# Optimization experiments

Measured on AMD Instinct MI355X. Metric: run time of the kernel, lower is better.

Reference implementation:

```python
import jax, jax.numpy as jnp
import numpy as np

N_NODES = 20000
N_EDGES = 640000
HIDDEN = 128
HEADS = 8
HEAD_DIM = HIDDEN // HEADS
SCALE = HEAD_DIM ** -0.5
EPS = 1e-8


def setup_inputs() -> dict:
    key = jax.random.key(0)
    ks = jax.random.split(key, 12)
    s = HIDDEN ** -0.5
    return {
        "query": jax.random.normal(ks[0], (N_NODES, HIDDEN), jnp.float32),
        "key": jax.random.normal(ks[1], (N_NODES, HIDDEN), jnp.float32),
        "value": jax.random.normal(ks[2], (N_NODES, HIDDEN), jnp.float32),
        "edge_index": jax.random.randint(ks[3], (2, N_EDGES), 0, N_NODES, jnp.int64 if jax.config.jax_enable_x64 else jnp.int32),
        "Wq": jax.random.normal(ks[4], (HIDDEN, HIDDEN), jnp.float32) * s,
        "bq": jax.random.normal(ks[5], (HIDDEN,), jnp.float32) * s,
        "Wk": jax.random.normal(ks[6], (HIDDEN, HIDDEN), jnp.float32) * s,
        "bk": jax.random.normal(ks[7], (HIDDEN,), jnp.float32) * s,
        "Wv": jax.random.normal(ks[8], (HIDDEN, HIDDEN), jnp.float32) * s,
        "bv": jax.random.normal(ks[9], (HIDDEN,), jnp.float32) * s,
        "Wo": jax.random.normal(ks[10], (HIDDEN, HIDDEN), jnp.float32) * s,
        "bo": jax.random.normal(ks[11], (HIDDEN,), jnp.float32) * s,
    }


def reference(query, key, value, edge_index, Wq, bq, Wk, bk, Wv, bv, Wo, bo):
    n = query.shape[0]
    # projections (torch nn.Linear: x @ W.T + b)
    Q = (query @ Wq.T + bq).reshape(n, HEADS, HEAD_DIM)
    K = (key @ Wk.T + bk).reshape(n, HEADS, HEAD_DIM)
    V = (value @ Wv.T + bv).reshape(n, HEADS, HEAD_DIM)

    src, dst = edge_index[0], edge_index[1]
    # per-edge, per-head scores: [E, H]
    scores = jnp.einsum('ehd,ehd->eh', Q[dst], K[src]) * SCALE
    # segment softmax over incoming edges of each dst node
    seg_max = jax.ops.segment_max(scores, dst, num_segments=n)  # [N, H]
    seg_max = jnp.where(jnp.isfinite(seg_max), seg_max, 0.0)
    exp_scores = jnp.exp(scores - seg_max[dst])
    seg_sum = jax.ops.segment_sum(exp_scores, dst, num_segments=n)  # [N, H]
    attn = exp_scores / (seg_sum[dst] + EPS)  # [E, H]

    # scatter-weighted aggregation of V[src] into dst
    weighted = attn[:, :, None] * V[src]  # [E, H, D]
    out = jax.ops.segment_sum(weighted, dst, num_segments=n)  # [N, H, D]
    out = out.reshape(n, HIDDEN)
    return out @ Wo.T + bo
```

## Files before the change

### kernel.cpp

```cpp
#include <hip/hip_runtime.h>
#include <math.h>

#define NN 20000
#define NE 640000
#define HID 128
#define NH 8
#define HD 16
#define ATT_SCALE 0.25f

#define EPB 4096
#define NBLK1 157
#define NBUCK 157
#define SCAN_N (NBUCK * NBLK1)
#define SPT 25
#define PCHUNK 79

typedef __attribute__((ext_vector_type(8))) short bhalf8;
typedef __attribute__((ext_vector_type(4))) float floatx4;

__device__ __forceinline__ short f2b(float f) {
  union { float f; unsigned u; } a;
  a.f = f;
  unsigned r = a.u + 0x7FFF + ((a.u >> 16) & 1);
  return (short)(r >> 16);
}

__device__ __forceinline__ float b2f(short s) {
  union { unsigned u; float f; } a;
  a.u = ((unsigned)(unsigned short)s) << 16;
  return a.f;
}

__device__ __forceinline__ bhalf8 load_a8(const float* __restrict__ p) {
  float4 x0 = *(const float4*)p;
  float4 x1 = *(const float4*)(p + 4);
  bhalf8 a;
  a[0] = f2b(x0.x); a[1] = f2b(x0.y); a[2] = f2b(x0.z); a[3] = f2b(x0.w);
  a[4] = f2b(x1.x); a[5] = f2b(x1.y); a[6] = f2b(x1.z); a[7] = f2b(x1.w);
  return a;
}

__global__ __launch_bounds__(256) void k_hist_wconv(
    const int* __restrict__ dst, int* __restrict__ cnt1,
    const float* __restrict__ W0, const float* __restrict__ W1,
    const float* __restrict__ W2, const float* __restrict__ W3,
    short* __restrict__ out) {
  int t = threadIdx.x, b = blockIdx.x;
  if (b < NBLK1) {
    __shared__ int h[NBUCK];
    for (int i = t; i < NBUCK; i += 256) h[i] = 0;
    __syncthreads();
    const int4* d4 = (const int4*)dst;
    int q0 = (b * EPB) >> 2;
#pragma unroll
    for (int it = 0; it < EPB / 1024; ++it) {
      int i4 = q0 + it * 256 + t;
      if (i4 < NE / 4) {
        int4 d = d4[i4];
        atomicAdd(&h[d.x >> 7], 1);
        atomicAdd(&h[d.y >> 7], 1);
        atomicAdd(&h[d.z >> 7], 1);
        atomicAdd(&h[d.w >> 7], 1);
      }
    }
    __syncthreads();
    for (int i = t; i < NBUCK; i += 256) cnt1[i * NBLK1 + b] = h[i];
  } else {
    int i = (b - NBLK1) * 1024 + t * 4;
    int m = i >> 14;
    const float* src = (m == 0) ? W0 : (m == 1) ? W1 : (m == 2) ? W2 : W3;
    float4 x = *(const float4*)(src + (i & 16383));
    short4 o;
    o.x = f2b(x.x); o.y = f2b(x.y); o.z = f2b(x.z); o.w = f2b(x.w);
    *(short4*)(out + i) = o;
  }
}

template <int STRIDE, int HALF>
__device__ __forceinline__ void gemm_mfma(const float* __restrict__ X,
                                          const short* __restrict__ Wb,
                                          const float* __restrict__ B,
                                          short* __restrict__ O, int wrow) {
  int lane = threadIdx.x & 63;
  int rr = lane & 15;
  int g = lane >> 4;
  int arow = wrow + rr;
  floatx4 acc[8];
#pragma unroll
  for (int nt = 0; nt < 8; ++nt) acc[nt] = (floatx4){0.f, 0.f, 0.f, 0.f};
#pragma unroll
  for (int kt = 0; kt < 4; ++kt) {
    bhalf8 a;
    if (arow < NN) {
      a = load_a8(X + (size_t)arow * HID + kt * 32 + g * 8);
    } else {
      a = (bhalf8){0, 0, 0, 0, 0, 0, 0, 0};
    }
#pragma unroll
    for (int nt = 0; nt < 8; ++nt) {
      bhalf8 b = *(const bhalf8*)(Wb + (nt * 16 + rr) * HID + kt * 32 + g * 8);
      acc[nt] = __builtin_amdgcn_mfma_f32_16x16x32_bf16(a, b, acc[nt], 0, 0, 0);
    }
  }
  int orow0 = wrow + g * 4;
#pragma unroll
  for (int nt = 0; nt < 8; ++nt) {
    int col = nt * 16 + rr;
    float bias = B[col];
#pragma unroll
    for (int i = 0; i < 4; ++i) {
      int r = orow0 + i;
      if (r < NN) {
        O[((size_t)(nt >> 1) * NN + r) * STRIDE + HALF + (nt & 1) * 16 + rr] =
            f2b(acc[nt][i] + bias);
      }
    }
  }
}

__global__ __launch_bounds__(1024) void k_scan_proj(
    int* __restrict__ cnt1, int* __restrict__ boff,
    const float* __restrict__ q, const float* __restrict__ k,
    const float* __restrict__ v, const short* __restrict__ Wb,
    const float* __restrict__ bq, const float* __restrict__ bk,
    const float* __restrict__ bv, short* __restrict__ Qh,
    short* __restrict__ KVh) {
  __shared__ int sa[1024], sb[1024];
  int t = threadIdx.x;
  if (blockIdx.x == 0) {
    int base = t * SPT;
    int s = 0;
#pragma unroll 5
    for (int u = 0; u < SPT; ++u) {
      int i = base + u;
      s += (i < SCAN_N) ? cnt1[i] : 0;
    }
    sa[t] = s;
    __syncthreads();
    int* sp = sa;
    int* dp = sb;
    for (int st = 1; st < 1024; st <<= 1) {
      dp[t] = sp[t] + (t >= st ? sp[t - st] : 0);
      __syncthreads();
      int* tmp = sp; sp = dp; dp = tmp;
    }
    int run = sp[t] - s;
#pragma unroll 5
    for (int u = 0; u < SPT; ++u) {
      int i = base + u;
      if (i < SCAN_N) {
        int vv = cnt1[i];
        cnt1[i] = run;
        run += vv;
      }
    }
    __syncthreads();
    for (int i = t; i < NBUCK; i += 1024) boff[i] = cnt1[i * NBLK1];
    if (t == 0) boff[NBUCK] = NE;
  } else {
    int b = blockIdx.x - 1;
    int mat = b / PCHUNK;
    int wrow = (b % PCHUNK) * 256 + (t >> 6) * 16;
    if (mat == 0) gemm_mfma<32, 0>(q, Wb, bq, Qh, wrow);
    else if (mat == 1) gemm_mfma<64, 0>(k, Wb + 16384, bk, KVh, wrow);
    else gemm_mfma<64, 32>(v, Wb + 2 * 16384, bv, KVh, wrow);
  }
}

__global__ __launch_bounds__(256) void k_p1scat(const int* __restrict__ src,
                                                const int* __restrict__ dst,
                                                const int* __restrict__ cnt1,
                                                int* __restrict__ tmp) {
  __shared__ int cur[NBUCK];
  int t = threadIdx.x, b = blockIdx.x;
  for (int i = t; i < NBUCK; i += 256) cur[i] = cnt1[i * NBLK1 + b];
  __syncthreads();
  const int4* s4 = (const int4*)src;
  const int4* d4 = (const int4*)dst;
  int q0 = (b * EPB) >> 2;
#pragma unroll
  for (int it = 0; it < EPB / 1024; ++it) {
    int i4 = q0 + it * 256 + t;
    if (i4 < NE / 4) {
      int4 s = s4[i4];
      int4 d = d4[i4];
      int p;
      p = atomicAdd(&cur[d.x >> 7], 1); tmp[p] = (s.x << 7) | (d.x & 127);
      p = atomicAdd(&cur[d.y >> 7], 1); tmp[p] = (s.y << 7) | (d.y & 127);
      p = atomicAdd(&cur[d.z >> 7], 1); tmp[p] = (s.z << 7) | (d.z & 127);
      p = atomicAdd(&cur[d.w >> 7], 1); tmp[p] = (s.w << 7) | (d.w & 127);
    }
  }
}

__global__ __launch_bounds__(128, 4) void k_edge(
    const int* __restrict__ tmp, const int* __restrict__ boff,
    const short* __restrict__ Qh, const short* __restrict__ KVh,
    const short* __restrict__ Wb, const float* __restrict__ bo,
    float* __restrict__ O) {
  __shared__ int hits[512];
  __shared__ int els[512];
  __shared__ short att[8][136];
  __shared__ int h8[8], c8[8], o8[8];
  __shared__ int nhit;
  int t = threadIdx.x;
  int bx = blockIdx.x;
  int b = bx >> 4;
  int l0 = (bx & 15) * 8;
  int node0 = 8 * bx;
  if (t < 8) h8[t] = 0;
  if (t == 0) nhit = 0;
  __syncthreads();
  int lo = boff[b], hi = boff[b + 1];
  const int4* t4 = (const int4*)tmp;
  int q0i = lo >> 2, q1i = (hi + 3) >> 2;
  for (int i4 = q0i + t; i4 < q1i; i4 += 128) {
    int4 w4 = t4[i4];
    int e = 4 * i4;
#pragma unroll
    for (int u = 0; u < 4; ++u) {
      int w = (u == 0) ? w4.x : (u == 1) ? w4.y : (u == 2) ? w4.z : w4.w;
      int ei = e + u;
      if (ei >= lo && ei < hi) {
        unsigned rel = (unsigned)((w & 127) - l0);
        if (rel < 8u) {
          int p = atomicAdd(&nhit, 1);
          if (p < 512) hits[p] = w;
          atomicAdd(&h8[rel], 1);
        }
      }
    }
  }
  __syncthreads();
  if (t == 0) {
    int r = 0;
#pragma unroll
    for (int u = 0; u < 8; ++u) {
      o8[u] = r;
      c8[u] = r;
      r += h8[u];
    }
  }
  __syncthreads();
  int n = nhit < 512 ? nhit : 512;
  for (int i = t; i < n; i += 128) {
    int w = hits[i];
    int p = atomicAdd(&c8[(w & 127) - l0], 1);
    els[p] = w >> 7;
  }
  __syncthreads();
  int nl = t >> 4;
  int node = node0 + nl;
  int sub = t & 15;
  int j = sub >> 2;
  int r = sub & 3;
  int i0 = o8[nl];
  int i1 = i0 + h8[nl];
  bool valid = node < NN;
#pragma unroll
  for (int hp = 0; hp < 4; ++hp) {
    float qf[8];
    if (valid) {
      bhalf8 qv = *(const bhalf8*)(Qh + ((size_t)hp * NN + node) * 32 + r * 8);
#pragma unroll
      for (int u = 0; u < 8; ++u) qf[u] = b2f(qv[u]);
    } else {
#pragma unroll
      for (int u = 0; u < 8; ++u) qf[u] = 0.f;
    }
    float l = 0.f;
    float acc[8];
#pragma unroll
    for (int u = 0; u < 8; ++u) acc[u] = 0.f;
    int i = i0 + j;
    for (; i + 4 < i1; i += 8) {
      int s1 = els[i], s2 = els[i + 4];
      const short* b1 = KVh + ((size_t)hp * NN + s1) * 64;
      const short* b2 = KVh + ((size_t)hp * NN + s2) * 64;
      bhalf8 kc1 = *(const bhalf8*)(b1 + r * 8);
      bhalf8 vc1 = *(const bhalf8*)(b1 + 32 + r * 8);
      bhalf8 kc2 = *(const bhalf8*)(b2 + r * 8);
      bhalf8 vc2 = *(const bhalf8*)(b2 + 32 + r * 8);
      float d1 = 0.f, d2 = 0.f;
#pragma unroll
      for (int u = 0; u < 8; ++u) {
        d1 += qf[u] * b2f(kc1[u]);
        d2 += qf[u] * b2f(kc2[u]);
      }
      d1 += __shfl_xor(d1, 1, 64);
      d2 += __shfl_xor(d2, 1, 64);
      float p1 = __expf(d1 * ATT_SCALE);
      float p2 = __expf(d2 * ATT_SCALE);
      l += p1 + p2;
#pragma unroll
      for (int u = 0; u < 8; ++u) acc[u] += p1 * b2f(vc1[u]) + p2 * b2f(vc2[u]);
    }
    if (i < i1) {
      int s1 = els[i];
      const short* b1 = KVh + ((size_t)hp * NN + s1) * 64;
      bhalf8 kc1 = *(const bhalf8*)(b1 + r * 8);
      bhalf8 vc1 = *(const bhalf8*)(b1 + 32 + r * 8);
      float d1 = 0.f;
#pragma unroll
      for (int u = 0; u < 8; ++u) d1 += qf[u] * b2f(kc1[u]);
      d1 += __shfl_xor(d1, 1, 64);
      float p1 = __expf(d1 * ATT_SCALE);
      l += p1;
#pragma unroll
      for (int u = 0; u < 8; ++u) acc[u] += p1 * b2f(vc1[u]);
    }
#pragma unroll
    for (int mask = 4; mask <= 8; mask <<= 1) {
      l += __shfl_xor(l, mask, 64);
#pragma unroll
      for (int u = 0; u < 8; ++u) acc[u] += __shfl_xor(acc[u], mask, 64);
    }
    float inv = 1.f / (l + 1e-8f);
    if (j == 0) {
      bhalf8 st;
#pragma unroll
      for (int u = 0; u < 8; ++u) st[u] = f2b(acc[u] * inv);
      *(bhalf8*)(&att[nl][hp * 32 + r * 8]) = st;
    }
  }
  __syncthreads();
  int w = t >> 6;
  int plane = t & 63;
  int rr = plane & 15;
  int pg = plane >> 4;
  const short* Wo = Wb + 3 * 16384;
  floatx4 oacc[4];
#pragma unroll
  for (int ntl = 0; ntl < 4; ++ntl) oacc[ntl] = (floatx4){0.f, 0.f, 0.f, 0.f};
#pragma unroll
  for (int kt = 0; kt < 4; ++kt) {
    bhalf8 a;
    if (rr < 8 && node0 + rr < NN) {
      a = *(const bhalf8*)(&att[rr][kt * 32 + pg * 8]);
    } else {
      a = (bhalf8){0, 0, 0, 0, 0, 0, 0, 0};
    }
#pragma unroll
    for (int ntl = 0; ntl < 4; ++ntl) {
      int nt = w * 4 + ntl;
      bhalf8 bb = *(const bhalf8*)(Wo + (nt * 16 + rr) * HID + kt * 32 + pg * 8);
      oacc[ntl] = __builtin_amdgcn_mfma_f32_16x16x32_bf16(a, bb, oacc[ntl], 0, 0, 0);
    }
  }
#pragma unroll
  for (int ntl = 0; ntl < 4; ++ntl) {
    int col = (w * 4 + ntl) * 16 + rr;
    float bias = bo[col];
#pragma unroll
    for (int ii = 0; ii < 4; ++ii) {
      int rw = pg * 4 + ii;
      if (rw < 8 && node0 + rw < NN) {
        O[(size_t)(node0 + rw) * HID + col] = oacc[ntl][ii] + bias;
      }
    }
  }
}

extern "C" void kernel_launch(void* const* d_in, const int* in_sizes, int n_in,
                              void* d_out, int out_size, void* d_ws,
                              size_t ws_size, hipStream_t stream) {
  const float* q = (const float*)d_in[0];
  const float* k = (const float*)d_in[1];
  const float* v = (const float*)d_in[2];
  const int* ei = (const int*)d_in[3];
  const float* Wq = (const float*)d_in[4];
  const float* bq = (const float*)d_in[5];
  const float* Wk = (const float*)d_in[6];
  const float* bk = (const float*)d_in[7];
  const float* Wv = (const float*)d_in[8];
  const float* bv = (const float*)d_in[9];
  const float* Wo = (const float*)d_in[10];
  const float* bo = (const float*)d_in[11];
  const int* src = ei;
  const int* dst = ei + NE;

  int* tmp = (int*)d_ws;
  int* cnt1 = tmp + NE;
  int* boff = cnt1 + 24704;
  short* Wb = (short*)(boff + 160);
  short* Qh = Wb + 4 * 16384;
  short* KVh = Qh + NN * HID;
  float* O = (float*)d_out;

  k_hist_wconv<<<NBLK1 + 64, 256, 0, stream>>>(dst, cnt1, Wq, Wk, Wv, Wo, Wb);
  k_scan_proj<<<1 + 3 * PCHUNK, 1024, 0, stream>>>(cnt1, boff, q, k, v, Wb, bq,
                                                   bk, bv, Qh, KVh);
  k_p1scat<<<NBLK1, 256, 0, stream>>>(src, dst, cnt1, tmp);
  k_edge<<<NBUCK * 16, 128, 0, stream>>>(tmp, boff, Qh, KVh, Wb, bo, O);
}
```

Baseline: 98.23 us.

## Bin edges by destination octet so each edge block reads only its own edges

Changes the counting sort from 128-node buckets to 8-node bins, matching the per-block node group of the edge kernel. A new column-scan kernel computes per-bin offsets across histogram blocks, and the edge kernel reads its contiguous edge range directly instead of filtering a shared bucket. This removes the redundant scanning of each large bucket by sixteen blocks. It adds a larger histogram in shared memory and global memory, plus an extra launch whose serial per-bin loop reads memory with a stride.

```diff
diff --git a/kernel.cpp b/kernel.cpp
--- a/kernel.cpp
+++ b/kernel.cpp
@@ -10,9 +10,8 @@
 
 #define EPB 4096
 #define NBLK1 157
-#define NBUCK 157
-#define SCAN_N (NBUCK * NBLK1)
-#define SPT 25
+#define FBIN 2500
+#define SPT2 3
 #define PCHUNK 79
 
 typedef __attribute__((ext_vector_type(8))) short bhalf8;
@@ -47,8 +46,8 @@
     short* __restrict__ out) {
   int t = threadIdx.x, b = blockIdx.x;
   if (b < NBLK1) {
-    __shared__ int h[NBUCK];
-    for (int i = t; i < NBUCK; i += 256) h[i] = 0;
+    __shared__ int h[FBIN];
+    for (int i = t; i < FBIN; i += 256) h[i] = 0;
     __syncthreads();
     const int4* d4 = (const int4*)dst;
     int q0 = (b * EPB) >> 2;
@@ -57,14 +56,14 @@
       int i4 = q0 + it * 256 + t;
       if (i4 < NE / 4) {
         int4 d = d4[i4];
-        atomicAdd(&h[d.x >> 7], 1);
-        atomicAdd(&h[d.y >> 7], 1);
-        atomicAdd(&h[d.z >> 7], 1);
-        atomicAdd(&h[d.w >> 7], 1);
+        atomicAdd(&h[d.x >> 3], 1);
+        atomicAdd(&h[d.y >> 3], 1);
+        atomicAdd(&h[d.z >> 3], 1);
+        atomicAdd(&h[d.w >> 3], 1);
       }
     }
     __syncthreads();
-    for (int i = t; i < NBUCK; i += 256) cnt1[i * NBLK1 + b] = h[i];
+    for (int i = t; i < FBIN; i += 256) cnt1[i * NBLK1 + b] = h[i];
   } else {
     int i = (b - NBLK1) * 1024 + t * 4;
     int m = i >> 14;
@@ -74,6 +73,21 @@
     o.x = f2b(x.x); o.y = f2b(x.y); o.z = f2b(x.z); o.w = f2b(x.w);
     *(short4*)(out + i) = o;
   }
+}
+
+__global__ __launch_bounds__(256) void k_colscan(int* __restrict__ cnt1,
+                                                 int* __restrict__ tot) {
+  int bin = blockIdx.x * 256 + threadIdx.x;
+  if (bin >= FBIN) return;
+  int base = bin * NBLK1;
+  int run = 0;
+#pragma unroll 4
+  for (int b = 0; b < NBLK1; ++b) {
+    int v = cnt1[base + b];
+    cnt1[base + b] = run;
+    run += v;
+  }
+  tot[bin] = run;
 }
 
 template <int STRIDE, int HALF>
@@ -119,7 +133,7 @@
 }
 
 __global__ __launch_bounds__(1024) void k_scan_proj(
-    int* __restrict__ cnt1, int* __restrict__ boff,
+    const int* __restrict__ tot, int* __restrict__ binstart,
     const float* __restrict__ q, const float* __restrict__ k,
     const float* __restrict__ v, const short* __restrict__ Wb,
     const float* __restrict__ bq, const float* __restrict__ bk,
@@ -128,12 +142,12 @@
   __shared__ int sa[1024], sb[1024];
   int t = threadIdx.x;
   if (blockIdx.x == 0) {
-    int base = t * SPT;
+    int base = t * SPT2;
     int s = 0;
-#pragma unroll 5
-    for (int u = 0; u < SPT; ++u) {
+#pragma unroll
+    for (int u = 0; u < SPT2; ++u) {
       int i = base + u;
-      s += (i < SCAN_N) ? cnt1[i] : 0;
+      s += (i < FBIN) ? tot[i] : 0;
     }
     sa[t] = s;
     __syncthreads();
@@ -145,18 +159,15 @@
       int* tmp = sp; sp = dp; dp = tmp;
     }
     int run = sp[t] - s;
-#pragma unroll 5
-    for (int u = 0; u < SPT; ++u) {
+#pragma unroll
+    for (int u = 0; u < SPT2; ++u) {
       int i = base + u;
-      if (i < SCAN_N) {
-        int vv = cnt1[i];
-        cnt1[i] = run;
-        run += vv;
-      }
-    }
-    __syncthreads();
-    for (int i = t; i < NBUCK; i += 1024) boff[i] = cnt1[i * NBLK1];
-    if (t == 0) boff[NBUCK] = NE;
+      if (i < FBIN) {
+        binstart[i] = run;
+        run += tot[i];
+      }
+    }
+    if (t == 0) binstart[FBIN] = NE;
   } else {
     int b = blockIdx.x - 1;
     int mat = b / PCHUNK;
@@ -170,10 +181,11 @@
 __global__ __launch_bounds__(256) void k_p1scat(const int* __restrict__ src,
                                                 const int* __restrict__ dst,
                                                 const int* __restrict__ cnt1,
+                                                const int* __restrict__ binstart,
                                                 int* __restrict__ tmp) {
-  __shared__ int cur[NBUCK];
+  __shared__ int cur[FBIN];
   int t = threadIdx.x, b = blockIdx.x;
-  for (int i = t; i < NBUCK; i += 256) cur[i] = cnt1[i * NBLK1 + b];
+  for (int i = t; i < FBIN; i += 256) cur[i] = cnt1[i * NBLK1 + b] + binstart[i];
   __syncthreads();
   const int4* s4 = (const int4*)src;
   const int4* d4 = (const int4*)dst;
@@ -185,35 +197,33 @@
       int4 s = s4[i4];
       int4 d = d4[i4];
       int p;
-      p = atomicAdd(&cur[d.x >> 7], 1); tmp[p] = (s.x << 7) | (d.x & 127);
-      p = atomicAdd(&cur[d.y >> 7], 1); tmp[p] = (s.y << 7) | (d.y & 127);
-      p = atomicAdd(&cur[d.z >> 7], 1); tmp[p] = (s.z << 7) | (d.z & 127);
-      p = atomicAdd(&cur[d.w >> 7], 1); tmp[p] = (s.w << 7) | (d.w & 127);
+      p = atomicAdd(&cur[d.x >> 3], 1); tmp[p] = (s.x << 3) | (d.x & 7);
+      p = atomicAdd(&cur[d.y >> 3], 1); tmp[p] = (s.y << 3) | (d.y & 7);
+      p = atomicAdd(&cur[d.z >> 3], 1); tmp[p] = (s.z << 3) | (d.z & 7);
+      p = atomicAdd(&cur[d.w >> 3], 1); tmp[p] = (s.w << 3) | (d.w & 7);
     }
   }
 }
 
 __global__ __launch_bounds__(128, 4) void k_edge(
-    const int* __restrict__ tmp, const int* __restrict__ boff,
+    const int* __restrict__ tmp, const int* __restrict__ binstart,
     const short* __restrict__ Qh, const short* __restrict__ KVh,
     const short* __restrict__ Wb, const float* __restrict__ bo,
     float* __restrict__ O) {
-  __shared__ int hits[512];
+  __shared__ int raw[512];
   __shared__ int els[512];
   __shared__ short att[8][136];
   __shared__ int h8[8], c8[8], o8[8];
-  __shared__ int nhit;
   int t = threadIdx.x;
   int bx = blockIdx.x;
-  int b = bx >> 4;
-  int l0 = (bx & 15) * 8;
   int node0 = 8 * bx;
   if (t < 8) h8[t] = 0;
-  if (t == 0) nhit = 0;
-  __syncthreads();
-  int lo = boff[b], hi = boff[b + 1];
+  __syncthreads();
+  int lo = binstart[bx], hi = binstart[bx + 1];
+  int cnt = hi - lo;
+  if (cnt > 512) cnt = 512;
   const int4* t4 = (const int4*)tmp;
-  int q0i = lo >> 2, q1i = (hi + 3) >> 2;
+  int q0i = lo >> 2, q1i = (lo + cnt + 3) >> 2;
   for (int i4 = q0i + t; i4 < q1i; i4 += 128) {
     int4 w4 = t4[i4];
     int e = 4 * i4;
@@ -221,13 +231,10 @@
     for (int u = 0; u < 4; ++u) {
       int w = (u == 0) ? w4.x : (u == 1) ? w4.y : (u == 2) ? w4.z : w4.w;
       int ei = e + u;
-      if (ei >= lo && ei < hi) {
-        unsigned rel = (unsigned)((w & 127) - l0);
-        if (rel < 8u) {
-          int p = atomicAdd(&nhit, 1);
-          if (p < 512) hits[p] = w;
-          atomicAdd(&h8[rel], 1);
-        }
+      int pos = ei - lo;
+      if (pos >= 0 && pos < cnt) {
+        raw[pos] = w;
+        atomicAdd(&h8[w & 7], 1);
       }
     }
   }
@@ -242,11 +249,10 @@
     }
   }
   __syncthreads();
-  int n = nhit < 512 ? nhit : 512;
-  for (int i = t; i < n; i += 128) {
-    int w = hits[i];
-    int p = atomicAdd(&c8[(w & 127) - l0], 1);
-    els[p] = w >> 7;
+  for (int i = t; i < cnt; i += 128) {
+    int w = raw[i];
+    int p = atomicAdd(&c8[w & 7], 1);
+    els[p] = w >> 3;
   }
   __syncthreads();
   int nl = t >> 4;
@@ -381,15 +387,17 @@
 
   int* tmp = (int*)d_ws;
   int* cnt1 = tmp + NE;
-  int* boff = cnt1 + 24704;
-  short* Wb = (short*)(boff + 160);
+  int* tot = cnt1 + 392512;
+  int* binstart = tot + 2512;
+  short* Wb = (short*)(binstart + 2512);
   short* Qh = Wb + 4 * 16384;
   short* KVh = Qh + NN * HID;
   float* O = (float*)d_out;
 
   k_hist_wconv<<<NBLK1 + 64, 256, 0, stream>>>(dst, cnt1, Wq, Wk, Wv, Wo, Wb);
-  k_scan_proj<<<1 + 3 * PCHUNK, 1024, 0, stream>>>(cnt1, boff, q, k, v, Wb, bq,
-                                                   bk, bv, Qh, KVh);
-  k_p1scat<<<NBLK1, 256, 0, stream>>>(src, dst, cnt1, tmp);
-  k_edge<<<NBUCK * 16, 128, 0, stream>>>(tmp, boff, Qh, KVh, Wb, bo, O);
-}
+  k_colscan<<<(FBIN + 255) / 256, 256, 0, stream>>>(cnt1, tot);
+  k_scan_proj<<<1 + 3 * PCHUNK, 1024, 0, stream>>>(tot, binstart, q, k, v, Wb,
+                                                   bq, bk, bv, Qh, KVh);
+  k_p1scat<<<NBLK1, 256, 0, stream>>>(src, dst, cnt1, binstart, tmp);
+  k_edge<<<FBIN, 128, 0, stream>>>(tmp, binstart, Qh, KVh, Wb, bo, O);
+}
```

After: 131.0 us. 1.33x slower.
